# Optimization experiments

Hardware: AMD Instinct MI355X
Metric: run time of the kernel (lower is better)

## Reference

```python
import jax, jax.numpy as jnp
import numpy as np

B = 512
T = 64
D_MODEL = 1024
N_HEADS = 16
DH = D_MODEL // N_HEADS
GRID_H, GRID_W = 8, 8
DX_MAX, DY_MAX = GRID_W - 1, GRID_H - 1
NUM_REL = (2 * DX_MAX + 1) * (2 * DY_MAX + 1)  # 225


def _build_rel_index():
    # Exactly mirrors RelSelfAttention2DShaw._build_rel_index for an 8x8 board.
    yy, xx = np.meshgrid(np.arange(GRID_H), np.arange(GRID_W), indexing='ij')
    coords = np.stack([xx.reshape(-1), yy.reshape(-1)], axis=-1)  # [T, 2] (x, y)
    disp = coords[None, :, :] - coords[:, None, :]                # [T, T, 2]
    dx = np.clip(disp[..., 0], -DX_MAX, DX_MAX) + DX_MAX
    dy = np.clip(disp[..., 1], -DY_MAX, DY_MAX) + DY_MAX
    return (dx + (2 * DX_MAX + 1) * dy).astype(np.int32)          # [T, T]


def setup_inputs() -> dict:
    key = jax.random.key(0)
    ks = jax.random.split(key, 12)
    w_std = 0.02
    inp = {
        'x':    jax.random.normal(ks[0], (B, T, D_MODEL), dtype=jnp.float32),
        'Wq_w': jax.random.normal(ks[1], (D_MODEL, D_MODEL), dtype=jnp.float32) * w_std,
        'Wq_b': jax.random.normal(ks[2], (D_MODEL,), dtype=jnp.float32) * w_std,
        'Wk_w': jax.random.normal(ks[3], (D_MODEL, D_MODEL), dtype=jnp.float32) * w_std,
        'Wk_b': jax.random.normal(ks[4], (D_MODEL,), dtype=jnp.float32) * w_std,
        'Wv_w': jax.random.normal(ks[5], (D_MODEL, D_MODEL), dtype=jnp.float32) * w_std,
        'Wv_b': jax.random.normal(ks[6], (D_MODEL,), dtype=jnp.float32) * w_std,
        'Wo_w': jax.random.normal(ks[7], (D_MODEL, D_MODEL), dtype=jnp.float32) * w_std,
        'Wo_b': jax.random.normal(ks[8], (D_MODEL,), dtype=jnp.float32) * w_std,
        'rel_q': jax.random.normal(ks[9],  (N_HEADS, NUM_REL, DH), dtype=jnp.float32) * w_std,
        'rel_k': jax.random.normal(ks[10], (N_HEADS, NUM_REL, DH), dtype=jnp.float32) * w_std,
        'rel_v': jax.random.normal(ks[11], (N_HEADS, NUM_REL, DH), dtype=jnp.float32) * w_std,
        'rel_index': jnp.asarray(_build_rel_index()),
    }
    return inp


def reference(x, Wq_w, Wq_b, Wk_w, Wk_b, Wv_w, Wv_b, Wo_w, Wo_b,
              rel_q, rel_k, rel_v, rel_index):
    Bc, Tc, D = x.shape
    H, dh = N_HEADS, DH
    scale = 1.0 / jnp.sqrt(jnp.asarray(dh, dtype=x.dtype))

    # Projections (nn.Linear uses y = x @ W.T + b), split into heads: [B, H, T, dh]
    q = (x @ Wq_w.T + Wq_b).reshape(Bc, Tc, H, dh).transpose(0, 2, 1, 3)
    k = (x @ Wk_w.T + Wk_b).reshape(Bc, Tc, H, dh).transpose(0, 2, 1, 3)
    v = (x @ Wv_w.T + Wv_b).reshape(Bc, Tc, H, dh).transpose(0, 2, 1, 3)

    # Gather per-displacement relative embeddings: [H, T, T, dh]
    rq = rel_q[:, rel_index]
    rk = rel_k[:, rel_index]
    rv = rel_v[:, rel_index]

    # e_ij = (q_i + aQ_ij) . (k_j + aK_ij) / sqrt(dh), expanded into 4 terms
    qk = jnp.einsum('bhtd,bhsd->bhts', q, k)
    q_relk = jnp.einsum('bhtd,htsd->bhts', q, rk)
    relq_k = jnp.einsum('htsd,bhsd->bhts', rq, k)
    relq_relk = jnp.einsum('htsd,htsd->hts', rq, rk)
    logits = (qk + q_relk + relq_k + relq_relk[None]) * scale

    attn = jax.nn.softmax(logits, axis=-1)  # [B, H, T, T]

    # z_i = sum_j attn_ij * (v_j + aV_ij)
    out_v = jnp.einsum('bhts,bhsd->bhtd', attn, v)
    out_relv = jnp.einsum('bhts,htsd->bhtd', attn, rv)
    out = (out_v + out_relv).transpose(0, 2, 1, 3).reshape(Bc, Tc, D)
    return out @ Wo_w.T + Wo_b


if __name__ == '__main__':
    y = reference(**setup_inputs())
    print(y.shape, y.dtype)
```

## Files before the change

kernel.cpp:

```cpp
#include <hip/hip_runtime.h>
#include <cstdint>


typedef unsigned short u16;
typedef unsigned int u32;
typedef __bf16 bf16x8 __attribute__((ext_vector_type(8)));
typedef float f32x4 __attribute__((ext_vector_type(4)));

#define MFMA16(a, b, c) __builtin_amdgcn_mfma_f32_16x16x32_bf16(a, b, c, 0, 0, 0)
#define BAR __builtin_amdgcn_s_barrier()
#define SB __builtin_amdgcn_sched_barrier(0)
#define LGK(n) do { asm volatile("s_waitcnt lgkmcnt(" #n ")" ::: "memory"); SB; } while (0)
#define VMC(n) asm volatile("s_waitcnt vmcnt(" #n ")" ::: "memory")

__device__ __forceinline__ u16 f2bf(float f) {
  u32 u = __builtin_bit_cast(u32, f);
  u = (u + 0x7FFFu + ((u >> 16) & 1u)) >> 16;
  return (u16)u;
}
__device__ __forceinline__ float bf2f(u16 h) {
  return __builtin_bit_cast(float, ((u32)h) << 16);
}

__device__ __forceinline__ void g2l16(const void* g, void* lds_wave_base) {
#if __has_builtin(__builtin_amdgcn_global_load_lds)
  __builtin_amdgcn_global_load_lds(
      (const __attribute__((address_space(1))) u32*)(uintptr_t)g,
      (__attribute__((address_space(3))) u32*)(uintptr_t)lds_wave_base, 16, 0, 0);
#else
  uint4 v = *(const uint4*)g;
  *(uint4*)((char*)lds_wave_base + (threadIdx.x & 63) * 16) = v;
#endif
}

__global__ __launch_bounds__(256) void k_cvt(const float* __restrict__ src,
                                             u16* __restrict__ dst, int nq) {
  int i = blockIdx.x * 256 + threadIdx.x;
  if (i >= nq) return;
  float4 v = ((const float4*)src)[i];
  ushort4 o;
  o.x = f2bf(v.x); o.y = f2bf(v.y); o.z = f2bf(v.z); o.w = f2bf(v.w);
  ((ushort4*)dst)[i] = o;
}


template <int OFF, int KK>
__device__ __forceinline__ void rdAk(const char* lds, const int* abase,
                                     bf16x8 (&f)[4]) {
#pragma unroll
  for (int m = 0; m < 4; m++)
    f[m] = *(const bf16x8*)(lds + abase[KK] + OFF + m * 2048);
}
template <int OFF, int KK>
__device__ __forceinline__ void rdBk(const char* lds, const int* bbase,
                                     bf16x8 (&f)[2]) {
#pragma unroll
  for (int n = 0; n < 2; n++)
    f[n] = *(const bf16x8*)(lds + bbase[KK] + OFF + n * 2048);
}
__device__ __forceinline__ void mq8(f32x4 (&acc)[8][4], const bf16x8 (&af)[4],
                                    const bf16x8 (&bf)[2], int MR, int NC) {
#pragma unroll
  for (int m = 0; m < 4; m++)
#pragma unroll
    for (int n = 0; n < 2; n++)
      acc[MR + m][NC + n] = MFMA16(af[m], bf[n], acc[MR + m][NC + n]);
}
__device__ __forceinline__ void st2(const char* p0, const char* p1, int off,
                                    char* lds, int dst, int woff) {
  g2l16(p0 + off, lds + dst + woff);
  g2l16(p1 + off, lds + dst + 8192 + woff);
}

__device__ __forceinline__ void gemm256_core(const u16* __restrict__ A,
                                             const u16* __restrict__ Bm,
                                             int row0, int col0, char* lds,
                                             f32x4 (&acc)[8][4], int tid) {
  const int lane = tid & 63, w = tid >> 6;
  const int wr = w >> 2, wc = w & 3;
  const int l15 = lane & 15, l4 = lane >> 4;
  const int l7 = l15 & 7;
  int abase[2], bbase[2];
#pragma unroll
  for (int kk = 0; kk < 2; kk++) {
    int swz = ((kk * 4 + l4) ^ l7) << 4;
    abase[kk] = wr * 8192 + l15 * 128 + swz;
    bbase[kk] = 65536 + wc * 4096 + l15 * 128 + swz;
  }
  const int sub0 = tid >> 3, sl0 = tid & 7;
  const int sub1 = (512 + tid) >> 3, sl1 = tid & 7;
  const int woff = w * 1024;
  const char* pa0 = (const char*)A + (size_t)row0 * 2048 +
      (size_t)((sub0 & 63) | ((sub0 & 64) << 1)) * 2048 + (sl0 ^ (sub0 & 7)) * 16;
  const char* pa1 = (const char*)A + (size_t)row0 * 2048 +
      (size_t)((sub1 & 63) | ((sub1 & 64) << 1)) * 2048 + (sl1 ^ (sub1 & 7)) * 16;
  const char* pb0 = (const char*)Bm + (size_t)col0 * 2048 +
      (size_t)((sub0 & 31) | ((sub0 & 0x60) << 1)) * 2048 + (sl0 ^ (sub0 & 7)) * 16;
  const char* pb1 = (const char*)Bm + (size_t)col0 * 2048 +
      (size_t)((sub1 & 31) | ((sub1 & 0x60) << 1)) * 2048 + (sl1 ^ (sub1 & 7)) * 16;

  bf16x8 afA0[4], afA1[4], afC0[4], afC1[4], bfB0[2], bfB1[2];

  st2(pa0, pa1, 0, lds, 0, woff);
  st2(pb0, pb1, 0, lds, 65536, woff);
  st2(pa0, pa1, 131072, lds, 16384, woff);
  st2(pb0, pb1, 65536, lds, 65536 + 16384, woff);
  st2(pb0, pb1, 128, lds, 65536 + 32768, woff);
  st2(pa0, pa1, 131072 + 128, lds, 49152, woff);
  VMC(0);
  BAR;

  for (int u = 0; u < 7; ++u) {
    const int kB = u * 256;
    rdAk<0, 0>(lds, abase, afA0); rdBk<0, 0>(lds, bbase, bfB0);
    rdAk<0, 1>(lds, abase, afA1); rdBk<0, 1>(lds, bbase, bfB1);
    st2(pa0, pa1, kB + 128, lds, 32768, woff);
    BAR; LGK(6);
    __builtin_amdgcn_s_setprio(1);
    mq8(acc, afA0, bfB0, 0, 0);
    LGK(0);
    mq8(acc, afA1, bfB1, 0, 0);
    __builtin_amdgcn_s_setprio(0);
    BAR;
    rdAk<16384, 0>(lds, abase, afC0);
    rdAk<16384, 1>(lds, abase, afC1);
    st2(pb0, pb1, 65536 + kB + 128, lds, 65536 + 49152, woff);
    BAR; LGK(4);
    __builtin_amdgcn_s_setprio(1);
    mq8(acc, afC0, bfB0, 4, 0);
    LGK(0);
    mq8(acc, afC1, bfB1, 4, 0);
    __builtin_amdgcn_s_setprio(0);
    BAR;
    rdBk<16384, 0>(lds, bbase, bfB0);
    rdBk<16384, 1>(lds, bbase, bfB1);
    st2(pb0, pb1, kB + 256, lds, 65536, woff);
    st2(pa0, pa1, 131072 + kB + 256, lds, 16384, woff);
    BAR; LGK(2);
    __builtin_amdgcn_s_setprio(1);
    mq8(acc, afC0, bfB0, 4, 2); mq8(acc, afA0, bfB0, 0, 2);
    LGK(0);
    mq8(acc, afC1, bfB1, 4, 2); mq8(acc, afA1, bfB1, 0, 2);
    __builtin_amdgcn_s_setprio(0);
    VMC(6); BAR;
    rdAk<32768, 0>(lds, abase, afA0); rdBk<32768, 0>(lds, bbase, bfB0);
    rdAk<32768, 1>(lds, abase, afA1); rdBk<32768, 1>(lds, bbase, bfB1);
    st2(pa0, pa1, kB + 256, lds, 0, woff);
    BAR; LGK(6);
    __builtin_amdgcn_s_setprio(1);
    mq8(acc, afA0, bfB0, 0, 0);
    LGK(0);
    mq8(acc, afA1, bfB1, 0, 0);
    __builtin_amdgcn_s_setprio(0);
    BAR;
    rdAk<49152, 0>(lds, abase, afC0);
    rdAk<49152, 1>(lds, abase, afC1);
    st2(pb0, pb1, 65536 + kB + 256, lds, 65536 + 16384, woff);
    BAR; LGK(4);
    __builtin_amdgcn_s_setprio(1);
    mq8(acc, afC0, bfB0, 4, 0);
    LGK(0);
    mq8(acc, afC1, bfB1, 4, 0);
    __builtin_amdgcn_s_setprio(0);
    VMC(8); BAR;
    rdBk<49152, 0>(lds, bbase, bfB0);
    rdBk<49152, 1>(lds, bbase, bfB1);
    st2(pb0, pb1, kB + 384, lds, 65536 + 32768, woff);
    st2(pa0, pa1, 131072 + kB + 384, lds, 49152, woff);
    BAR; LGK(2);
    __builtin_amdgcn_s_setprio(1);
    mq8(acc, afC0, bfB0, 4, 2); mq8(acc, afA0, bfB0, 0, 2);
    LGK(0);
    mq8(acc, afC1, bfB1, 4, 2); mq8(acc, afA1, bfB1, 0, 2);
    __builtin_amdgcn_s_setprio(0);
    VMC(4); BAR;
  }
  {
    rdAk<0, 0>(lds, abase, afA0); rdBk<0, 0>(lds, bbase, bfB0);
    rdAk<0, 1>(lds, abase, afA1); rdBk<0, 1>(lds, bbase, bfB1);
    st2(pa0, pa1, 1792 + 128, lds, 32768, woff);
    BAR; LGK(6);
    mq8(acc, afA0, bfB0, 0, 0);
    LGK(0);
    mq8(acc, afA1, bfB1, 0, 0);
    BAR;
    rdAk<16384, 0>(lds, abase, afC0);
    rdAk<16384, 1>(lds, abase, afC1);
    st2(pb0, pb1, 65536 + 1792 + 128, lds, 65536 + 49152, woff);
    BAR; LGK(4);
    mq8(acc, afC0, bfB0, 4, 0);
    LGK(0);
    mq8(acc, afC1, bfB1, 4, 0);
    BAR;
    rdBk<16384, 0>(lds, bbase, bfB0);
    rdBk<16384, 1>(lds, bbase, bfB1);
    BAR; LGK(2);
    mq8(acc, afC0, bfB0, 4, 2); mq8(acc, afA0, bfB0, 0, 2);
    LGK(0);
    mq8(acc, afC1, bfB1, 4, 2); mq8(acc, afA1, bfB1, 0, 2);
    VMC(2); BAR;
    rdAk<32768, 0>(lds, abase, afA0); rdBk<32768, 0>(lds, bbase, bfB0);
    rdAk<32768, 1>(lds, abase, afA1); rdBk<32768, 1>(lds, bbase, bfB1);
    BAR; LGK(6);
    mq8(acc, afA0, bfB0, 0, 0);
    LGK(0);
    mq8(acc, afA1, bfB1, 0, 0);
    BAR;
    rdAk<49152, 0>(lds, abase, afC0);
    rdAk<49152, 1>(lds, abase, afC1);
    BAR; LGK(4);
    mq8(acc, afC0, bfB0, 4, 0);
    LGK(0);
    mq8(acc, afC1, bfB1, 4, 0);
    VMC(0); BAR;
    rdBk<49152, 0>(lds, bbase, bfB0);
    rdBk<49152, 1>(lds, bbase, bfB1);
    BAR; LGK(2);
    mq8(acc, afC0, bfB0, 4, 2); mq8(acc, afA0, bfB0, 0, 2);
    LGK(0);
    mq8(acc, afC1, bfB1, 4, 2); mq8(acc, afA1, bfB1, 0, 2);
    BAR;
  }
}

__global__ __launch_bounds__(512, 2) void k_gemm_qkv(
    const u16* __restrict__ A, const u16* __restrict__ Bm,
    const float* __restrict__ bq, const float* __restrict__ bk,
    const float* __restrict__ bv, u16* __restrict__ Qb, u16* __restrict__ Kb,
    u16* __restrict__ Vb) {
  __shared__ char lds[131072];
  const int tid = threadIdx.x;
  const int lane = tid & 63, w = tid >> 6;
  const int wr = w >> 2, wc = w & 3;
  const int l15 = lane & 15, l4 = lane >> 4;
  int f = blockIdx.x;
  int swz = (f & 7) * 192 + (f >> 3);
  int bcol = swz % 12, brow = swz / 12;
  const int row0 = brow * 256, col0 = bcol * 256;
  f32x4 acc[8][4] = {};
  gemm256_core(A, Bm, row0, col0, lds, acc, tid);
  char* eb = lds + w * 16384;
  const int colW = col0 + wc * 64;
  const int sel = colW >> 10, hd = colW & 1023;
  const int h = hd >> 6;
  const float* bp = (sel == 0) ? bq : (sel == 1) ? bk : bv;
  const float* biasW = bp + hd;
  u16* dstW = (sel == 0) ? Qb : (sel == 1) ? Kb : Vb;
#pragma unroll
  for (int r = 0; r < 4; r++) {
#pragma unroll
    for (int mm = 0; mm < 2; mm++) {
      int mf = r * 2 + mm;
#pragma unroll
      for (int nf = 0; nf < 4; nf++)
#pragma unroll
        for (int j = 0; j < 4; j++) {
          int rowl = mm * 16 + l4 * 4 + j;
          *(float*)(eb + rowl * 272 + (nf * 16 + l15) * 4) = acc[mf][nf][j];
        }
    }
    LGK(0);
#pragma unroll
    for (int it = 0; it < 4; it++) {
      int u = it * 64 + lane;
      int rowl = u >> 3, ch = u & 7;
      float4 a0 = *(const float4*)(eb + rowl * 272 + ch * 32);
      float4 a1 = *(const float4*)(eb + rowl * 272 + ch * 32 + 16);
      float4 b0 = *(const float4*)(biasW + ch * 8);
      float4 b1 = *(const float4*)(biasW + ch * 8 + 4);
      uint4 pk;
      pk.x = (u32)f2bf(a0.x + b0.x) | ((u32)f2bf(a0.y + b0.y) << 16);
      pk.y = (u32)f2bf(a0.z + b0.z) | ((u32)f2bf(a0.w + b0.w) << 16);
      pk.z = (u32)f2bf(a1.x + b1.x) | ((u32)f2bf(a1.y + b1.y) << 16);
      pk.w = (u32)f2bf(a1.z + b1.z) | ((u32)f2bf(a1.w + b1.w) << 16);
      int row = row0 + wr * 128 + r * 32 + rowl;
      int b = row >> 6, t = row & 63;
      *(uint4*)(dstW + ((size_t)(b * 16 + h)) * 4096 + t * 64 + ch * 8) = pk;
    }
    LGK(0);
  }
}

__global__ __launch_bounds__(512, 2) void k_gemm_out(
    const u16* __restrict__ A, const u16* __restrict__ Bm,
    const float* __restrict__ bo, float* __restrict__ out) {
  __shared__ char lds[131072];
  const int tid = threadIdx.x;
  const int lane = tid & 63, w = tid >> 6;
  const int wr = w >> 2, wc = w & 3;
  const int l15 = lane & 15, l4 = lane >> 4;
  int f = blockIdx.x;
  int swz = (f & 7) * 64 + (f >> 3);
  int bcol = swz & 3, brow = swz >> 2;
  const int row0 = brow * 256, col0 = bcol * 256;
  f32x4 acc[8][4] = {};
  gemm256_core(A, Bm, row0, col0, lds, acc, tid);
  char* eb = lds + w * 16384;
  const int colW = col0 + wc * 64;
  const float* biasW = bo + colW;
#pragma unroll
  for (int r = 0; r < 4; r++) {
#pragma unroll
    for (int mm = 0; mm < 2; mm++) {
      int mf = r * 2 + mm;
#pragma unroll
      for (int nf = 0; nf < 4; nf++)
#pragma unroll
        for (int j = 0; j < 4; j++) {
          int rowl = mm * 16 + l4 * 4 + j;
          *(float*)(eb + rowl * 272 + (nf * 16 + l15) * 4) = acc[mf][nf][j];
        }
    }
    LGK(0);
#pragma unroll
    for (int it = 0; it < 8; it++) {
      int u = it * 64 + lane;
      int rowl = u >> 4, ch = u & 15;
      float4 a0 = *(const float4*)(eb + rowl * 272 + ch * 16);
      float4 b0 = *(const float4*)(biasW + ch * 4);
      a0.x += b0.x; a0.y += b0.y; a0.z += b0.z; a0.w += b0.w;
      int row = row0 + wr * 128 + r * 32 + rowl;
      *(float4*)(out + (size_t)row * 1024 + colW + ch * 4) = a0;
    }
    LGK(0);
  }
}

__global__ __launch_bounds__(256) void k_bias1(
    const u16* __restrict__ Qb, const u16* __restrict__ relq,
    const u16* __restrict__ relk, const int* __restrict__ relidx,
    u16* __restrict__ bias1) {
  const int tid = threadIdx.x, lane = tid & 63, w = tid >> 6;
  const int l15 = lane & 15, l4 = lane >> 4;
  const int t = blockIdx.x, h = blockIdx.y, bc = blockIdx.z;
  __shared__ char lds[16640];
  char* RK = lds;
  char* RQ = lds + 8192;
  float* T3 = (float*)(lds + 16384);
#pragma unroll
  for (int c = 0; c < 2; c++) {
    int ch = c * 256 + tid;
    int sr = ch >> 3, sl = (ch & 7) ^ (sr & 7);
    int ri = relidx[t * 64 + sr];
    size_t so = ((size_t)h * 225 + ri) * 64 + sl * 8;
    g2l16(relk + so, RK + c * 4096 + w * 1024);
    g2l16(relq + so, RQ + c * 4096 + w * 1024);
  }
  __syncthreads();
  if (tid < 64) {
    int sr = tid;
    float sum = 0.f;
#pragma unroll
    for (int sl = 0; sl < 8; sl++) {
      int o = sr * 128 + ((sl ^ (sr & 7)) << 4);
      bf16x8 aq = *(const bf16x8*)(RQ + o);
      bf16x8 ak = *(const bf16x8*)(RK + o);
#pragma unroll
      for (int j = 0; j < 8; j++) sum += (float)aq[j] * (float)ak[j];
    }
    T3[sr] = sum;
  }
  bf16x8 bfr[4][2];
#pragma unroll
  for (int n = 0; n < 4; n++)
#pragma unroll
    for (int kh = 0; kh < 2; kh++) {
      int r = n * 16 + l15;
      int sl = ((kh << 2) + l4) ^ (r & 7);
      bfr[n][kh] = *(const bf16x8*)(RK + r * 128 + sl * 16);
    }
  __syncthreads();
  f32x4 acc[4][4] = {};
#pragma unroll
  for (int m = 0; m < 4; m++) {
    int bb = bc * 256 + w * 64 + m * 16 + l15;
    const u16* ap = Qb + ((size_t)(bb * 16 + h)) * 4096 + t * 64 + l4 * 8;
    bf16x8 a0 = *(const bf16x8*)ap;
    bf16x8 a1 = *(const bf16x8*)(ap + 32);
#pragma unroll
    for (int n = 0; n < 4; n++) {
      acc[m][n] = MFMA16(a0, bfr[n][0], acc[m][n]);
      acc[m][n] = MFMA16(a1, bfr[n][1], acc[m][n]);
    }
  }
#pragma unroll
  for (int m = 0; m < 4; m++)
#pragma unroll
    for (int n = 0; n < 4; n++)
#pragma unroll
      for (int j = 0; j < 4; j++) {
        int bb = bc * 256 + w * 64 + m * 16 + l4 * 4 + j;
        int s_ = n * 16 + l15;
        bias1[((size_t)(bb * 16 + h)) * 4096 + t * 64 + s_] =
            f2bf(acc[m][n][j] + T3[s_]);
      }
}

__global__ __launch_bounds__(256) void k_bias2(
    const u16* __restrict__ Kb, const u16* __restrict__ relq,
    const int* __restrict__ relidx, u16* __restrict__ bias2) {
  const int tid = threadIdx.x, lane = tid & 63, w = tid >> 6;
  const int l15 = lane & 15, l4 = lane >> 4;
  const int s = blockIdx.x, h = blockIdx.y, bc = blockIdx.z;
  __shared__ char lds[8192];
#pragma unroll
  for (int c = 0; c < 2; c++) {
    int ch = c * 256 + tid;
    int tq = ch >> 3, sl = (ch & 7) ^ (tq & 7);
    int ri = relidx[tq * 64 + s];
    g2l16(relq + ((size_t)h * 225 + ri) * 64 + sl * 8,
          lds + c * 4096 + w * 1024);
  }
  __syncthreads();
  bf16x8 bfr[4][2];
#pragma unroll
  for (int n = 0; n < 4; n++)
#pragma unroll
    for (int kh = 0; kh < 2; kh++) {
      int r = n * 16 + l15;
      int sl = ((kh << 2) + l4) ^ (r & 7);
      bfr[n][kh] = *(const bf16x8*)(lds + r * 128 + sl * 16);
    }
  f32x4 acc[4][4] = {};
#pragma unroll
  for (int m = 0; m < 4; m++) {
    int bb = bc * 256 + w * 64 + m * 16 + l15;
    const u16* ap = Kb + ((size_t)(bb * 16 + h)) * 4096 + s * 64 + l4 * 8;
    bf16x8 a0 = *(const bf16x8*)ap;
    bf16x8 a1 = *(const bf16x8*)(ap + 32);
#pragma unroll
    for (int n = 0; n < 4; n++) {
      acc[m][n] = MFMA16(a0, bfr[n][0], acc[m][n]);
      acc[m][n] = MFMA16(a1, bfr[n][1], acc[m][n]);
    }
  }
#pragma unroll
  for (int m = 0; m < 4; m++)
#pragma unroll
    for (int n = 0; n < 4; n++)
#pragma unroll
      for (int j = 0; j < 4; j++) {
        int bb = bc * 256 + w * 64 + m * 16 + l4 * 4 + j;
        int tcol = n * 16 + l15;
        bias2[((size_t)(bb * 16 + h)) * 4096 + s * 64 + tcol] =
            f2bf(acc[m][n][j]);
      }
}

__global__ __launch_bounds__(256) void k_attn(
    const u16* __restrict__ Qb, const u16* __restrict__ Kb,
    const u16* __restrict__ Vb, const u16* __restrict__ b1g,
    const u16* __restrict__ b2g, u16* __restrict__ Pg,
    u16* __restrict__ aout) {
  const int tid = threadIdx.x, lane = tid & 63, w = tid >> 6;
  const int l15 = lane & 15, l4 = lane >> 4;
  const int b = blockIdx.x, h = blockIdx.y;
  __shared__ char lds[49152];
  char* Qt = lds;
  char* Kt = lds + 8192;
  char* Vt = lds + 16384;
  char* B1 = lds + 24576;
  char* B2 = lds + 32768;
  char* Pt = lds + 40960;
  const size_t base = ((size_t)(b * 16 + h)) * 4096;
#pragma unroll
  for (int c = 0; c < 2; c++) {
    int ch = c * 256 + tid;
    int r = ch >> 3, sl = (ch & 7) ^ (r & 7);
    size_t so = base + r * 64 + sl * 8;
    int dst = c * 4096 + w * 1024;
    g2l16(Qb + so, Qt + dst);
    g2l16(Kb + so, Kt + dst);
    g2l16(Vb + so, Vt + dst);
    g2l16(b1g + so, B1 + dst);
    g2l16(b2g + so, B2 + dst);
  }
  __syncthreads();
  f32x4 acc[4] = {};
  bf16x8 qf[2];
  {
    int r = w * 16 + l15;
#pragma unroll
    for (int kh = 0; kh < 2; kh++) {
      int sl = ((kh << 2) + l4) ^ (r & 7);
      qf[kh] = *(const bf16x8*)(Qt + r * 128 + sl * 16);
    }
  }
#pragma unroll
  for (int n = 0; n < 4; n++) {
    int r = n * 16 + l15;
#pragma unroll
    for (int kh = 0; kh < 2; kh++) {
      int sl = ((kh << 2) + l4) ^ (r & 7);
      bf16x8 kf = *(const bf16x8*)(Kt + r * 128 + sl * 16);
      acc[n] = MFMA16(qf[kh], kf, acc[n]);
    }
  }
  const int t0 = w * 16 + l4 * 4;
#pragma unroll
  for (int j = 0; j < 4; j++) {
    int t_ = t0 + j;
    float lv[4];
#pragma unroll
    for (int n = 0; n < 4; n++) {
      int s_ = n * 16 + l15;
      float x = acc[n][j];
      x += bf2f(*(const u16*)(B1 + t_ * 128 + ((s_ * 2) ^ ((t_ & 7) << 4))));
      x += bf2f(*(const u16*)(B2 + s_ * 128 + ((t_ * 2) ^ ((s_ & 7) << 4))));
      lv[n] = x * 0.125f;
    }
    float mx = fmaxf(fmaxf(lv[0], lv[1]), fmaxf(lv[2], lv[3]));
#pragma unroll
    for (int d = 1; d < 16; d <<= 1) mx = fmaxf(mx, __shfl_xor(mx, d, 64));
    float e0 = __expf(lv[0] - mx), e1 = __expf(lv[1] - mx);
    float e2 = __expf(lv[2] - mx), e3 = __expf(lv[3] - mx);
    float sum = e0 + e1 + e2 + e3;
#pragma unroll
    for (int d = 1; d < 16; d <<= 1) sum += __shfl_xor(sum, d, 64);
    float inv = 1.0f / sum;
    float pe[4] = {e0 * inv, e1 * inv, e2 * inv, e3 * inv};
#pragma unroll
    for (int n = 0; n < 4; n++) {
      int s_ = n * 16 + l15;
      *(u16*)(Pt + t_ * 128 + ((s_ * 2) ^ ((t_ & 7) << 4))) = f2bf(pe[n]);
    }
  }
  __syncthreads();
#pragma unroll
  for (int c = 0; c < 2; c++) {
    int ch = c * 256 + tid;
    int r = ch >> 3, sl = ch & 7;
    uint4 v = *(const uint4*)(Pt + r * 128 + ((sl ^ (r & 7)) << 4));
    *((uint4*)(Pg + base) + ch) = v;
  }
  f32x4 acc2[4] = {};
  bf16x8 pf[2];
  {
    int r = w * 16 + l15;
#pragma unroll
    for (int kh = 0; kh < 2; kh++) {
      int sl = ((kh << 2) + l4) ^ (r & 7);
      pf[kh] = *(const bf16x8*)(Pt + r * 128 + sl * 16);
    }
  }
#pragma unroll
  for (int n = 0; n < 4; n++) {
#pragma unroll
    for (int kh = 0; kh < 2; kh++) {
      bf16x8 tmp;
#pragma unroll
      for (int j = 0; j < 8; j++) {
        int s_ = (kh << 5) + (l4 << 3) + j;
        int d_ = n * 16 + l15;
        u16 uu = *(const u16*)(Vt + s_ * 128 + ((d_ * 2) ^ ((s_ & 7) << 4)));
        tmp[j] = __builtin_bit_cast(__bf16, uu);
      }
      acc2[n] = MFMA16(pf[kh], tmp, acc2[n]);
    }
  }
#pragma unroll
  for (int n = 0; n < 4; n++)
#pragma unroll
    for (int j = 0; j < 4; j++) {
      int t_ = t0 + j, d_ = n * 16 + l15;
      aout[((size_t)(b * 64 + t_)) * 1024 + h * 64 + d_] = f2bf(acc2[n][j]);
    }
}

__global__ __launch_bounds__(256) void k_relv(
    const u16* __restrict__ Pg, const u16* __restrict__ relv,
    const int* __restrict__ relidx, u16* __restrict__ aout) {
  const int tid = threadIdx.x, lane = tid & 63, w = tid >> 6;
  const int l15 = lane & 15, l4 = lane >> 4;
  const int t = blockIdx.x, h = blockIdx.y, bc = blockIdx.z;
  __shared__ char lds[8192];
#pragma unroll
  for (int c = 0; c < 2; c++) {
    int ch = c * 256 + tid;
    int sr = ch >> 3, sl = (ch & 7) ^ (sr & 7);
    int ri = relidx[t * 64 + sr];
    g2l16(relv + ((size_t)h * 225 + ri) * 64 + sl * 8,
          lds + c * 4096 + w * 1024);
  }
  __syncthreads();
  bf16x8 bfr[4][2];
#pragma unroll
  for (int n = 0; n < 4; n++)
#pragma unroll
    for (int kh = 0; kh < 2; kh++) {
      bf16x8 tmp;
#pragma unroll
      for (int j = 0; j < 8; j++) {
        int s_ = (kh << 5) + (l4 << 3) + j;
        int d_ = n * 16 + l15;
        u16 u = *(const u16*)(lds + s_ * 128 + ((d_ * 2) ^ ((s_ & 7) << 4)));
        tmp[j] = __builtin_bit_cast(__bf16, u);
      }
      bfr[n][kh] = tmp;
    }
  f32x4 acc[4][4] = {};
#pragma unroll
  for (int m = 0; m < 4; m++) {
    int bb = bc * 256 + w * 64 + m * 16 + l15;
    const u16* ap = Pg + ((size_t)(bb * 16 + h)) * 4096 + t * 64 + l4 * 8;
    bf16x8 a0 = *(const bf16x8*)ap;
    bf16x8 a1 = *(const bf16x8*)(ap + 32);
#pragma unroll
    for (int n = 0; n < 4; n++) {
      acc[m][n] = MFMA16(a0, bfr[n][0], acc[m][n]);
      acc[m][n] = MFMA16(a1, bfr[n][1], acc[m][n]);
    }
  }
#pragma unroll
  for (int m = 0; m < 4; m++)
#pragma unroll
    for (int n = 0; n < 4; n++)
#pragma unroll
      for (int j = 0; j < 4; j++) {
        int bb = bc * 256 + w * 64 + m * 16 + l4 * 4 + j;
        int d_ = n * 16 + l15;
        size_t o = ((size_t)(bb * 64 + t)) * 1024 + h * 64 + d_;
        aout[o] = f2bf(bf2f(aout[o]) + acc[m][n][j]);
      }
}

extern "C" void kernel_launch(void* const* d_in, const int* in_sizes, int n_in,
                              void* d_out, int out_size, void* d_ws,
                              size_t ws_size, hipStream_t stream) {
  const float* x = (const float*)d_in[0];
  const float* Wq = (const float*)d_in[1];
  const float* bq = (const float*)d_in[2];
  const float* Wk = (const float*)d_in[3];
  const float* bk = (const float*)d_in[4];
  const float* Wv = (const float*)d_in[5];
  const float* bv = (const float*)d_in[6];
  const float* Wo = (const float*)d_in[7];
  const float* bo = (const float*)d_in[8];
  const float* rq = (const float*)d_in[9];
  const float* rk = (const float*)d_in[10];
  const float* rv = (const float*)d_in[11];
  const int* ridx = (const int*)d_in[12];
  float* out = (float*)d_out;

  char* ws = (char*)d_ws;
  const size_t MB = 1ull << 20;
  u16* xb = (u16*)(ws + 0);
  u16* Qb = (u16*)(ws + 64 * MB);
  u16* Kb = (u16*)(ws + 128 * MB);
  u16* Vb = (u16*)(ws + 192 * MB);
  u16* b1 = (u16*)(ws + 256 * MB);
  u16* b2 = (u16*)(ws + 320 * MB);
  u16* aout = (u16*)(ws + 384 * MB);
  u16* wqkv = (u16*)(ws + 448 * MB);
  u16* wo = (u16*)(ws + 454 * MB);
  u16* relq = (u16*)(ws + 456 * MB);
  u16* relk = (u16*)(ws + 457 * MB);
  u16* relv = (u16*)(ws + 458 * MB);
  u16* Pg = xb;

  k_cvt<<<32768, 256, 0, stream>>>(x, xb, 8388608);
  k_cvt<<<1024, 256, 0, stream>>>(Wq, wqkv, 262144);
  k_cvt<<<1024, 256, 0, stream>>>(Wk, wqkv + 1048576, 262144);
  k_cvt<<<1024, 256, 0, stream>>>(Wv, wqkv + 2097152, 262144);
  k_cvt<<<1024, 256, 0, stream>>>(Wo, wo, 262144);
  k_cvt<<<225, 256, 0, stream>>>(rq, relq, 57600);
  k_cvt<<<225, 256, 0, stream>>>(rk, relk, 57600);
  k_cvt<<<225, 256, 0, stream>>>(rv, relv, 57600);

  k_gemm_qkv<<<1536, 512, 0, stream>>>(xb, wqkv, bq, bk, bv, Qb, Kb, Vb);
  k_bias1<<<dim3(64, 16, 2), 256, 0, stream>>>(Qb, relq, relk, ridx, b1);
  k_bias2<<<dim3(64, 16, 2), 256, 0, stream>>>(Kb, relq, ridx, b2);
  k_attn<<<dim3(512, 16), 256, 0, stream>>>(Qb, Kb, Vb, b1, b2, Pg, aout);
  k_relv<<<dim3(64, 16, 2), 256, 0, stream>>>(Pg, relv, ridx, aout);
  k_gemm_out<<<512, 512, 0, stream>>>(aout, wo, bo, out);
}
```

Measured before the change: 534.4 us.

## Merge weight conversions and bias kernels, remap block order, drop sched barrier

Replaces seven separate conversion launches with one multi-segment kernel, and fuses the two relative-bias kernels into a single kernel that computes bias1 and then bias2 per block. The bias and relv kernels get a linear grid with an XCD-aware index remap so that consecutive blocks on one XCD share a head and its relative embeddings. It also removes the sched_barrier from the LDS wait macro, giving the compiler more freedom to schedule. The intent is to cut launch overhead and improve cache locality, at the cost of more serial work per fused block and possible reordering hazards around the waits.

```diff
diff --git a/kernel.cpp b/kernel.cpp
--- a/kernel.cpp
+++ b/kernel.cpp
@@ -9,8 +9,7 @@
 
 #define MFMA16(a, b, c) __builtin_amdgcn_mfma_f32_16x16x32_bf16(a, b, c, 0, 0, 0)
 #define BAR __builtin_amdgcn_s_barrier()
-#define SB __builtin_amdgcn_sched_barrier(0)
-#define LGK(n) do { asm volatile("s_waitcnt lgkmcnt(" #n ")" ::: "memory"); SB; } while (0)
+#define LGK(n) asm volatile("s_waitcnt lgkmcnt(" #n ")" ::: "memory")
 #define VMC(n) asm volatile("s_waitcnt vmcnt(" #n ")" ::: "memory")
 
 __device__ __forceinline__ u16 f2bf(float f) {
@@ -43,6 +42,30 @@
   ((ushort4*)dst)[i] = o;
 }
 
+__global__ __launch_bounds__(256) void k_cvt7(
+    const float* s0, const float* s1, const float* s2, const float* s3,
+    const float* s4, const float* s5, const float* s6, u16* d0, u16* d1,
+    u16* d2, u16* d3, u16* d4, u16* d5, u16* d6) {
+  int seg = blockIdx.y;
+  const float* s;
+  u16* d;
+  int nq;
+  switch (seg) {
+    case 0: s = s0; d = d0; nq = 262144; break;
+    case 1: s = s1; d = d1; nq = 262144; break;
+    case 2: s = s2; d = d2; nq = 262144; break;
+    case 3: s = s3; d = d3; nq = 262144; break;
+    case 4: s = s4; d = d4; nq = 57600; break;
+    case 5: s = s5; d = d5; nq = 57600; break;
+    default: s = s6; d = d6; nq = 57600; break;
+  }
+  int i = blockIdx.x * 256 + threadIdx.x;
+  if (i >= nq) return;
+  float4 v = ((const float4*)s)[i];
+  ushort4 o;
+  o.x = f2bf(v.x); o.y = f2bf(v.y); o.z = f2bf(v.z); o.w = f2bf(v.w);
+  ((ushort4*)d)[i] = o;
+}
 
 template <int OFF, int KK>
 __device__ __forceinline__ void rdAk(const char* lds, const int* abase,
@@ -326,13 +349,16 @@
   }
 }
 
-__global__ __launch_bounds__(256) void k_bias1(
-    const u16* __restrict__ Qb, const u16* __restrict__ relq,
-    const u16* __restrict__ relk, const int* __restrict__ relidx,
-    u16* __restrict__ bias1) {
+__global__ __launch_bounds__(256) void k_bias12(
+    const u16* __restrict__ Qb, const u16* __restrict__ Kb,
+    const u16* __restrict__ relq, const u16* __restrict__ relk,
+    const int* __restrict__ relidx, u16* __restrict__ bias1,
+    u16* __restrict__ bias2) {
   const int tid = threadIdx.x, lane = tid & 63, w = tid >> 6;
   const int l15 = lane & 15, l4 = lane >> 4;
-  const int t = blockIdx.x, h = blockIdx.y, bc = blockIdx.z;
+  int f = blockIdx.x;
+  int seq = (f & 7) * 256 + (f >> 3);
+  const int h = seq >> 7, bc = (seq >> 6) & 1, i = seq & 63;
   __shared__ char lds[16640];
   char* RK = lds;
   char* RQ = lds + 8192;
@@ -341,7 +367,7 @@
   for (int c = 0; c < 2; c++) {
     int ch = c * 256 + tid;
     int sr = ch >> 3, sl = (ch & 7) ^ (sr & 7);
-    int ri = relidx[t * 64 + sr];
+    int ri = relidx[i * 64 + sr];
     size_t so = ((size_t)h * 225 + ri) * 64 + sl * 8;
     g2l16(relk + so, RK + c * 4096 + w * 1024);
     g2l16(relq + so, RQ + c * 4096 + w * 1024);
@@ -360,91 +386,87 @@
     }
     T3[sr] = sum;
   }
-  bf16x8 bfr[4][2];
-#pragma unroll
-  for (int n = 0; n < 4; n++)
-#pragma unroll
-    for (int kh = 0; kh < 2; kh++) {
-      int r = n * 16 + l15;
-      int sl = ((kh << 2) + l4) ^ (r & 7);
-      bfr[n][kh] = *(const bf16x8*)(RK + r * 128 + sl * 16);
-    }
+  {
+    bf16x8 bfr[4][2];
+#pragma unroll
+    for (int n = 0; n < 4; n++)
+#pragma unroll
+      for (int kh = 0; kh < 2; kh++) {
+        int r = n * 16 + l15;
+        int sl = ((kh << 2) + l4) ^ (r & 7);
+        bfr[n][kh] = *(const bf16x8*)(RK + r * 128 + sl * 16);
+      }
+    __syncthreads();
+    f32x4 acc[4][4] = {};
+#pragma unroll
+    for (int m = 0; m < 4; m++) {
+      int bb = bc * 256 + w * 64 + m * 16 + l15;
+      const u16* ap = Qb + ((size_t)(bb * 16 + h)) * 4096 + i * 64 + l4 * 8;
+      bf16x8 a0 = *(const bf16x8*)ap;
+      bf16x8 a1 = *(const bf16x8*)(ap + 32);
+#pragma unroll
+      for (int n = 0; n < 4; n++) {
+        acc[m][n] = MFMA16(a0, bfr[n][0], acc[m][n]);
+        acc[m][n] = MFMA16(a1, bfr[n][1], acc[m][n]);
+      }
+    }
+#pragma unroll
+    for (int m = 0; m < 4; m++)
+#pragma unroll
+      for (int n = 0; n < 4; n++)
+#pragma unroll
+        for (int j = 0; j < 4; j++) {
+          int bb = bc * 256 + w * 64 + m * 16 + l4 * 4 + j;
+          int s_ = n * 16 + l15;
+          bias1[((size_t)(bb * 16 + h)) * 4096 + i * 64 + s_] =
+              f2bf(acc[m][n][j] + T3[s_]);
+        }
+  }
   __syncthreads();
-  f32x4 acc[4][4] = {};
-#pragma unroll
-  for (int m = 0; m < 4; m++) {
-    int bb = bc * 256 + w * 64 + m * 16 + l15;
-    const u16* ap = Qb + ((size_t)(bb * 16 + h)) * 4096 + t * 64 + l4 * 8;
-    bf16x8 a0 = *(const bf16x8*)ap;
-    bf16x8 a1 = *(const bf16x8*)(ap + 32);
-#pragma unroll
-    for (int n = 0; n < 4; n++) {
-      acc[m][n] = MFMA16(a0, bfr[n][0], acc[m][n]);
-      acc[m][n] = MFMA16(a1, bfr[n][1], acc[m][n]);
-    }
-  }
-#pragma unroll
-  for (int m = 0; m < 4; m++)
-#pragma unroll
-    for (int n = 0; n < 4; n++)
-#pragma unroll
-      for (int j = 0; j < 4; j++) {
-        int bb = bc * 256 + w * 64 + m * 16 + l4 * 4 + j;
-        int s_ = n * 16 + l15;
-        bias1[((size_t)(bb * 16 + h)) * 4096 + t * 64 + s_] =
-            f2bf(acc[m][n][j] + T3[s_]);
-      }
-}
-
-__global__ __launch_bounds__(256) void k_bias2(
-    const u16* __restrict__ Kb, const u16* __restrict__ relq,
-    const int* __restrict__ relidx, u16* __restrict__ bias2) {
-  const int tid = threadIdx.x, lane = tid & 63, w = tid >> 6;
-  const int l15 = lane & 15, l4 = lane >> 4;
-  const int s = blockIdx.x, h = blockIdx.y, bc = blockIdx.z;
-  __shared__ char lds[8192];
 #pragma unroll
   for (int c = 0; c < 2; c++) {
     int ch = c * 256 + tid;
     int tq = ch >> 3, sl = (ch & 7) ^ (tq & 7);
-    int ri = relidx[tq * 64 + s];
+    int ri = relidx[tq * 64 + i];
     g2l16(relq + ((size_t)h * 225 + ri) * 64 + sl * 8,
-          lds + c * 4096 + w * 1024);
+          RK + c * 4096 + w * 1024);
   }
   __syncthreads();
-  bf16x8 bfr[4][2];
-#pragma unroll
-  for (int n = 0; n < 4; n++)
-#pragma unroll
-    for (int kh = 0; kh < 2; kh++) {
-      int r = n * 16 + l15;
-      int sl = ((kh << 2) + l4) ^ (r & 7);
-      bfr[n][kh] = *(const bf16x8*)(lds + r * 128 + sl * 16);
-    }
-  f32x4 acc[4][4] = {};
-#pragma unroll
-  for (int m = 0; m < 4; m++) {
-    int bb = bc * 256 + w * 64 + m * 16 + l15;
-    const u16* ap = Kb + ((size_t)(bb * 16 + h)) * 4096 + s * 64 + l4 * 8;
-    bf16x8 a0 = *(const bf16x8*)ap;
-    bf16x8 a1 = *(const bf16x8*)(ap + 32);
-#pragma unroll
-    for (int n = 0; n < 4; n++) {
-      acc[m][n] = MFMA16(a0, bfr[n][0], acc[m][n]);
-      acc[m][n] = MFMA16(a1, bfr[n][1], acc[m][n]);
-    }
-  }
-#pragma unroll
-  for (int m = 0; m < 4; m++)
+  {
+    bf16x8 bfr[4][2];
 #pragma unroll
     for (int n = 0; n < 4; n++)
 #pragma unroll
-      for (int j = 0; j < 4; j++) {
-        int bb = bc * 256 + w * 64 + m * 16 + l4 * 4 + j;
-        int tcol = n * 16 + l15;
-        bias2[((size_t)(bb * 16 + h)) * 4096 + s * 64 + tcol] =
-            f2bf(acc[m][n][j]);
+      for (int kh = 0; kh < 2; kh++) {
+        int r = n * 16 + l15;
+        int sl = ((kh << 2) + l4) ^ (r & 7);
+        bfr[n][kh] = *(const bf16x8*)(RK + r * 128 + sl * 16);
       }
+    f32x4 acc[4][4] = {};
+#pragma unroll
+    for (int m = 0; m < 4; m++) {
+      int bb = bc * 256 + w * 64 + m * 16 + l15;
+      const u16* ap = Kb + ((size_t)(bb * 16 + h)) * 4096 + i * 64 + l4 * 8;
+      bf16x8 a0 = *(const bf16x8*)ap;
+      bf16x8 a1 = *(const bf16x8*)(ap + 32);
+#pragma unroll
+      for (int n = 0; n < 4; n++) {
+        acc[m][n] = MFMA16(a0, bfr[n][0], acc[m][n]);
+        acc[m][n] = MFMA16(a1, bfr[n][1], acc[m][n]);
+      }
+    }
+#pragma unroll
+    for (int m = 0; m < 4; m++)
+#pragma unroll
+      for (int n = 0; n < 4; n++)
+#pragma unroll
+        for (int j = 0; j < 4; j++) {
+          int bb = bc * 256 + w * 64 + m * 16 + l4 * 4 + j;
+          int tcol = n * 16 + l15;
+          bias2[((size_t)(bb * 16 + h)) * 4096 + i * 64 + tcol] =
+              f2bf(acc[m][n][j]);
+        }
+  }
 }
 
 __global__ __launch_bounds__(256) void k_attn(
@@ -572,7 +594,9 @@
     const int* __restrict__ relidx, u16* __restrict__ aout) {
   const int tid = threadIdx.x, lane = tid & 63, w = tid >> 6;
   const int l15 = lane & 15, l4 = lane >> 4;
-  const int t = blockIdx.x, h = blockIdx.y, bc = blockIdx.z;
+  int f = blockIdx.x;
+  int seq = (f & 7) * 256 + (f >> 3);
+  const int h = seq >> 7, bc = (seq >> 6) & 1, t = seq & 63;
   __shared__ char lds[8192];
 #pragma unroll
   for (int c = 0; c < 2; c++) {
@@ -659,18 +683,13 @@
   u16* Pg = xb;
 
   k_cvt<<<32768, 256, 0, stream>>>(x, xb, 8388608);
-  k_cvt<<<1024, 256, 0, stream>>>(Wq, wqkv, 262144);
-  k_cvt<<<1024, 256, 0, stream>>>(Wk, wqkv + 1048576, 262144);
-  k_cvt<<<1024, 256, 0, stream>>>(Wv, wqkv + 2097152, 262144);
-  k_cvt<<<1024, 256, 0, stream>>>(Wo, wo, 262144);
-  k_cvt<<<225, 256, 0, stream>>>(rq, relq, 57600);
-  k_cvt<<<225, 256, 0, stream>>>(rk, relk, 57600);
-  k_cvt<<<225, 256, 0, stream>>>(rv, relv, 57600);
+  k_cvt7<<<dim3(1024, 7), 256, 0, stream>>>(
+      Wq, Wk, Wv, Wo, rq, rk, rv, wqkv, wqkv + 1048576, wqkv + 2097152, wo,
+      relq, relk, relv);
 
   k_gemm_qkv<<<1536, 512, 0, stream>>>(xb, wqkv, bq, bk, bv, Qb, Kb, Vb);
-  k_bias1<<<dim3(64, 16, 2), 256, 0, stream>>>(Qb, relq, relk, ridx, b1);
-  k_bias2<<<dim3(64, 16, 2), 256, 0, stream>>>(Kb, relq, ridx, b2);
+  k_bias12<<<2048, 256, 0, stream>>>(Qb, Kb, relq, relk, ridx, b1, b2);
   k_attn<<<dim3(512, 16), 256, 0, stream>>>(Qb, Kb, Vb, b1, b2, Pg, aout);
-  k_relv<<<dim3(64, 16, 2), 256, 0, stream>>>(Pg, relv, ridx, aout);
+  k_relv<<<2048, 256, 0, stream>>>(Pg, relv, ridx, aout);
   k_gemm_out<<<512, 512, 0, stream>>>(aout, wo, bo, out);
 }
```

Measured after the change: 534.4 us. Within noise of the previous version (+0.0%).
